# Kernel optimization log

Hardware: AMD Instinct MI355X
Metric: run time of the kernel (lower is better)

## Reference

```python
import jax, jax.numpy as jnp
import numpy as np

N, E, EP = 200000, 1600000, 1000000
D, H1, CH, XDIM, L = 64, 256, 128, 20, 3


def gelu(x):
    return jax.nn.gelu(x, approximate=False)  # torch default = exact erf GELU


def dyt(x, w, b, a):
    # DynamicTanh (channels_last): w * tanh(alpha * x) + b
    return w * jnp.tanh(a * x) + b


def graph_norm(x, w, b, ms, eps=1e-5):
    # PyG GraphNorm with a single graph (batch = all zeros)
    mean = jnp.mean(x, axis=0, keepdims=True)
    xc = x - ms * mean
    var = jnp.mean(xc * xc, axis=0, keepdims=True)
    return w * xc / jnp.sqrt(var + eps) + b


def setup_inputs() -> dict:
    key = jax.random.key(0)
    ks = iter(jax.random.split(key, 64))
    nrm = lambda shape, s: jax.random.normal(next(ks), shape, jnp.float32) * s
    d = {}
    d['x_res'] = nrm((N, D), 1.0)
    s = 1.0 / np.sqrt(D)
    d['Wl'] = nrm((L, D, D), s); d['bl'] = jnp.zeros((L, D)); d['Wr'] = nrm((L, D, D), s)
    d['gn_w'] = jnp.ones((L, D)); d['gn_b'] = jnp.zeros((L, D)); d['gn_ms'] = jnp.ones((L, D))
    d['dyt1_w'] = jnp.ones((L * D,)); d['dyt1_b'] = jnp.zeros((L * D,)); d['dyt1_a'] = jnp.full((1,), 0.5, jnp.float32)
    d['lin1_w'] = nrm((L * D, H1), 1.0 / np.sqrt(L * D)); d['lin1_b'] = jnp.zeros((H1,))
    d['lin2_w'] = nrm((H1, H1), 1.0 / np.sqrt(H1)); d['lin2_b'] = jnp.zeros((H1,))
    d['lin3_w'] = nrm((H1, D), 1.0 / np.sqrt(H1)); d['lin3_b'] = jnp.zeros((D,))
    d['dyt2_w'] = jnp.ones((D,)); d['dyt2_b'] = jnp.zeros((D,)); d['dyt2_a'] = jnp.full((1,), 0.5, jnp.float32)
    d['adyt1_w'] = jnp.ones((2 * D,)); d['adyt1_b'] = jnp.zeros((2 * D,)); d['adyt1_a'] = jnp.full((1,), 0.5, jnp.float32)
    d['aa1_w'] = nrm((2 * D, H1), 1.0 / np.sqrt(2 * D)); d['aa1_b'] = jnp.zeros((H1,))
    d['aa2_w'] = nrm((H1, H1), 1.0 / np.sqrt(H1)); d['aa2_b'] = jnp.zeros((H1,))
    d['aa3_w'] = nrm((H1, H1), 1.0 / np.sqrt(H1)); d['aa3_b'] = jnp.zeros((H1,))
    d['adyt2_w'] = jnp.ones((H1,)); d['adyt2_b'] = jnp.zeros((H1,)); d['adyt2_a'] = jnp.full((1,), 0.5, jnp.float32)
    d['aa4_w'] = nrm((H1, XDIM), 1.0 / np.sqrt(H1)); d['aa4_b'] = jnp.zeros((XDIM,))
    d['c1_w'] = nrm((2 * D, CH), 1.0 / np.sqrt(2 * D)); d['c1_b'] = jnp.zeros((CH,))
    d['c2_w'] = nrm((CH, CH), 1.0 / np.sqrt(CH)); d['c2_b'] = jnp.zeros((CH,))
    d['c3_w'] = nrm((CH, 1), 1.0 / np.sqrt(CH)); d['c3_b'] = jnp.zeros((1,))
    d['edge_index'] = jax.random.randint(next(ks), (2, E), 0, N, dtype=jnp.int64 if jax.config.jax_enable_x64 else jnp.int32).astype(jnp.int32)
    d['contact_pred_index'] = jax.random.randint(next(ks), (2, EP), 0, N).astype(jnp.int32)
    return d


def reference(x_res, Wl, bl, Wr, gn_w, gn_b, gn_ms, dyt1_w, dyt1_b, dyt1_a,
              lin1_w, lin1_b, lin2_w, lin2_b, lin3_w, lin3_b, dyt2_w, dyt2_b, dyt2_a,
              adyt1_w, adyt1_b, adyt1_a, aa1_w, aa1_b, aa2_w, aa2_b, aa3_w, aa3_b,
              adyt2_w, adyt2_b, adyt2_a, aa4_w, aa4_b,
              c1_w, c1_b, c2_w, c2_b, c3_w, c3_b, edge_index, contact_pred_index):
    n = x_res.shape[0]
    src, dst = edge_index[0], edge_index[1]
    inz = x_res  # dropout is identity in eval / p~0
    x = x_res
    # in-degree for SAGE mean aggregation (clamped to 1 like PyG)
    deg = jnp.maximum(jax.ops.segment_sum(jnp.ones_like(src, dtype=x.dtype), dst, num_segments=n), 1.0)[:, None]
    xs = []
    for i in range(Wl.shape[0]):
        prev = x
        agg = jax.ops.segment_sum(x[src], dst, num_segments=n) / deg  # [N, D] mean of neighbor messages
        h = agg @ Wl[i] + bl[i] + x @ Wr[i]                            # SAGEConv: lin_l(aggr) + lin_r(x_dst)
        h = gelu(h)
        h = graph_norm(h, gn_w[i], gn_b[i], gn_ms[i])
        if i > 0:
            h = h + prev  # residual from layer 1 onward
        x = h
        xs.append(x)
    z = jnp.concatenate(xs, axis=1)  # JumpingKnowledge 'cat' -> [N, 3*D]
    z = dyt(z, dyt1_w, dyt1_b, dyt1_a)
    z = gelu(z @ lin1_w + lin1_b)
    z = gelu(z @ lin2_w + lin2_b)
    z = gelu(z @ lin3_w + lin3_b)
    z = dyt(z, dyt2_w, dyt2_b, dyt2_a)
    z = z + inz                                   # residual=True
    z = z / (jnp.linalg.norm(z, axis=1, keepdims=True) + 1e-10)  # normalize=True
    dec_in = jnp.concatenate([inz, z], axis=1)    # [N, 2*D]
    a = dyt(dec_in, adyt1_w, adyt1_b, adyt1_a)
    a = gelu(a @ aa1_w + aa1_b)
    a = gelu(a @ aa2_w + aa2_b)
    a = gelu(a @ aa3_w + aa3_b)
    a = dyt(a, adyt2_w, adyt2_b, adyt2_a)
    aa = jax.nn.log_softmax(a @ aa4_w + aa4_b, axis=1)  # [N, 20]
    ci, cj = contact_pred_index[0], contact_pred_index[1]
    ce = jnp.concatenate([z[ci], z[cj]], axis=1)  # [EP, 2*D] gather
    ce = gelu(ce @ c1_w + c1_b)
    ce = gelu(ce @ c2_w + c2_b)
    edge_probs = jax.nn.sigmoid((ce @ c3_w + c3_b)[:, 0])  # [EP]
    return aa, edge_probs
```

## Files before the change

### kernel.cpp

```cpp
#include <hip/hip_runtime.h>
#include <cstdint>
#include <cstddef>

constexpr int Nn  = 200000;
constexpr int Ee  = 1600000;
constexpr int EPp = 1000000;

typedef __attribute__((ext_vector_type(8))) short bf8_t;
typedef __attribute__((ext_vector_type(4))) float f4_t;

__device__ inline unsigned short f2bf(float f) {
  union { float f; unsigned u; } v; v.f = f;
  unsigned r = v.u + 0x7FFFu + ((v.u >> 16) & 1u);
  return (unsigned short)(r >> 16);
}
__device__ inline float bf2f(unsigned short u) {
  union { unsigned u; float f; } v; v.u = ((unsigned)u) << 16;
  return v.f;
}
__device__ inline float gelu_f(float v) {
  float u = v * fmaf(0.0356774081f, v * v, 0.7978845608f);
  float r = __builtin_amdgcn_rcpf(__expf(u + u) + 1.0f);
  return fmaf(-v, r, v);
}
__device__ inline float dyt_f(float x, float s2, float w, float b) {
  float r = __builtin_amdgcn_rcpf(__expf(s2 * x) + 1.0f);
  return fmaf(w, fmaf(-2.0f, r, 1.0f), b);
}


__global__ __launch_bounds__(256) void k_degi(const int* __restrict__ dst,
                                              int* __restrict__ cnt, int E) {
  int i = blockIdx.x * 256 + threadIdx.x;
  if (i < E) atomicAdd(&cnt[dst[i]], 1);
}

__global__ __launch_bounds__(256) void k_rdeg(const int* __restrict__ cnt,
                                              float* __restrict__ rdeg, int n) {
  int i = blockIdx.x * 256 + threadIdx.x;
  if (i < n) rdeg[i] = 1.0f / (float)(cnt[i] > 1 ? cnt[i] : 1);
}

__global__ __launch_bounds__(256) void k_scan1(const int* __restrict__ in,
                                               int* __restrict__ out,
                                               int* __restrict__ bsum, int n) {
  __shared__ int sd[256];
  int t = threadIdx.x;
  int base = blockIdx.x * 1024 + t * 4;
  int v[4]; int ts = 0;
  #pragma unroll
  for (int j = 0; j < 4; ++j) { v[j] = (base + j < n) ? in[base + j] : 0; ts += v[j]; }
  sd[t] = ts; __syncthreads();
  for (int off = 1; off < 256; off <<= 1) {
    int x = (t >= off) ? sd[t - off] : 0;
    __syncthreads();
    sd[t] += x;
    __syncthreads();
  }
  int excl = sd[t] - ts;
  #pragma unroll
  for (int j = 0; j < 4; ++j) { if (base + j < n) out[base + j] = excl; excl += v[j]; }
  if (t == 255) bsum[blockIdx.x] = sd[255];
}

__global__ void k_scan2(int* bsum, int nb) {
  __shared__ int sd[256];
  int t = threadIdx.x;
  int v = (t < nb) ? bsum[t] : 0;
  sd[t] = v; __syncthreads();
  for (int off = 1; off < 256; off <<= 1) {
    int x = (t >= off) ? sd[t - off] : 0;
    __syncthreads();
    sd[t] += x;
    __syncthreads();
  }
  if (t < nb) bsum[t] = sd[t] - v;
}

__global__ __launch_bounds__(256) void k_scan3(const int* __restrict__ part,
                                               const int* __restrict__ bsum,
                                               int* __restrict__ rowptr,
                                               int* __restrict__ cursor,
                                               int n, int total) {
  int i = blockIdx.x * 256 + threadIdx.x;
  if (i == 0) rowptr[n] = total;
  if (i < n) { int v = part[i] + bsum[i >> 10]; rowptr[i] = v; cursor[i] = v; }
}

__global__ __launch_bounds__(256) void k_fill(const int* __restrict__ src,
                                              const int* __restrict__ dst,
                                              int* __restrict__ cursor,
                                              int* __restrict__ colidx, int E) {
  int e = blockIdx.x * 256 + threadIdx.x;
  if (e >= E) return;
  int pos = atomicAdd(&cursor[dst[e]], 1);
  colidx[pos] = src[e];
}

__global__ __launch_bounds__(256) void k_gather(const unsigned short* __restrict__ x, int ldx,
                                                const int* __restrict__ rowptr,
                                                const int* __restrict__ colidx,
                                                const float* __restrict__ rdeg,
                                                unsigned short* __restrict__ agg, int n) {
  int wave = threadIdx.x >> 6, lane = threadIdx.x & 63;
  int node = blockIdx.x * 4 + wave;
  if (node >= n) return;
  int grp = lane >> 3, c = (lane & 7) * 8;
  int r0 = rowptr[node], r1 = rowptr[node + 1];
  float s[8] = {0.f, 0.f, 0.f, 0.f, 0.f, 0.f, 0.f, 0.f};
  for (int j = r0 + grp; j < r1; j += 8) {
    bf8_t v = *(const bf8_t*)(x + (size_t)colidx[j] * ldx + c);
    #pragma unroll
    for (int jj = 0; jj < 8; ++jj) s[jj] += bf2f((unsigned short)v[jj]);
  }
  #pragma unroll
  for (int jj = 0; jj < 8; ++jj) {
    s[jj] += __shfl_xor(s[jj], 8, 64);
    s[jj] += __shfl_xor(s[jj], 16, 64);
    s[jj] += __shfl_xor(s[jj], 32, 64);
  }
  if (grp == 0) {
    float r = rdeg[node];
    bf8_t o;
    #pragma unroll
    for (int jj = 0; jj < 8; ++jj) o[jj] = (short)f2bf(s[jj] * r);
    *(bf8_t*)(agg + (size_t)node * 64 + c) = o;
  }
}


__global__ __launch_bounds__(256) void k_cvt(const float* __restrict__ in,
                                             unsigned short* __restrict__ out, int n) {
  int i = blockIdx.x * 256 + threadIdx.x;
  if (i < n) out[i] = f2bf(in[i]);
}

__global__ __launch_bounds__(256) void k_wt2(const float* __restrict__ W,
                                             unsigned short* __restrict__ Wt,
                                             int K, int N, int total) {
  int i = blockIdx.x * 256 + threadIdx.x;
  if (i >= total) return;
  int n = i / K, k = i - n * K;
  float v = (n < N) ? W[(size_t)k * N + n] : 0.f;
  Wt[i] = f2bf(v);
}

__global__ __launch_bounds__(256) void k_wt3(const float* __restrict__ W,
                                             unsigned short* __restrict__ Wt,
                                             int Np, int Nr, int total) {
  int i = blockIdx.x * 256 + threadIdx.x;
  if (i >= total) return;
  int kin = i & 31;
  int j = i >> 5;
  int n = j % Np, kb = j / Np;
  int k = kb * 32 + kin;
  float v = (n < Nr) ? W[(size_t)k * Nr + n] : 0.f;
  Wt[i] = f2bf(v);
}

__global__ __launch_bounds__(256) void k_wtsage(const float* __restrict__ Wl,
                                                const float* __restrict__ Wr,
                                                unsigned short* __restrict__ Wt) {
  int i = blockIdx.x * 256 + threadIdx.x;
  if (i >= 3 * 64 * 128) return;
  int l = i >> 13, r = i & 8191, n = r >> 7, k = r & 127;
  float v = (k < 64) ? Wl[l * 4096 + k * 64 + n] : Wr[l * 4096 + (k - 64) * 64 + n];
  Wt[i] = f2bf(v);
}

__global__ __launch_bounds__(256) void k_stats(const float* __restrict__ h,
                                               float* __restrict__ stats, int n) {
  int lane = threadIdx.x & 63, grp = threadIdx.x >> 6;
  float s = 0.f, s2 = 0.f;
  for (int r = blockIdx.x * 4 + grp; r < n; r += gridDim.x * 4) {
    float v = h[(size_t)r * 64 + lane];
    s += v; s2 += v * v;
  }
  __shared__ float l1[4][64], l2[4][64];
  l1[grp][lane] = s; l2[grp][lane] = s2;
  __syncthreads();
  if (grp == 0) {
    s  = l1[0][lane] + l1[1][lane] + l1[2][lane] + l1[3][lane];
    s2 = l2[0][lane] + l2[1][lane] + l2[2][lane] + l2[3][lane];
    atomicAdd(&stats[lane], s);
    atomicAdd(&stats[64 + lane], s2);
  }
}

__global__ void k_statfin(float* stats, const float* __restrict__ ms_, int n) {
  int d = threadIdx.x;
  if (d < 64) {
    float invn = 1.0f / (float)n;
    float m  = stats[d] * invn;
    float e2 = stats[64 + d] * invn;
    float ms = ms_[d];
    float var = e2 - (2.0f * ms - ms * ms) * m * m;
    stats[128 + d] = ms * m;
    stats[192 + d] = rsqrtf(var + 1e-5f);
  }
}

__global__ __launch_bounds__(256) void k_norm(const float* __restrict__ h,
                                              const float* __restrict__ stats,
                                              const float* __restrict__ w,
                                              const float* __restrict__ b,
                                              unsigned short* __restrict__ zcol,
                                              const unsigned short* __restrict__ prev, int n) {
  int i = blockIdx.x * 256 + threadIdx.x;
  if (i >= n * 64) return;
  int r = i >> 6, d = i & 63;
  float v = (h[i] - stats[128 + d]) * stats[192 + d] * w[d] + b[d];
  if (prev) v += bf2f(prev[(size_t)r * 192 + d]);
  zcol[(size_t)r * 192 + d] = f2bf(v);
}

template <int NT>
__global__ __launch_bounds__(256) void mgemm(
    const void* __restrict__ A1, int lda1,
    const void* __restrict__ A2, int lda2, int K1, int a_bf16,
    const unsigned short* __restrict__ Wt,
    const float* __restrict__ bias,
    void* __restrict__ Cout, int ldc, int c_bf16, int act,
    int M, int K, int N) {
  int lane = threadIdx.x & 63, wave = threadIdx.x >> 6;
  int quad = lane >> 4, col = lane & 15;
  int row0 = blockIdx.x * 128 + wave * 32;
  int n_base = blockIdx.y * NT * 16;

  f4_t acc[2][NT];
  #pragma unroll
  for (int mt = 0; mt < 2; ++mt)
    #pragma unroll
    for (int nt = 0; nt < NT; ++nt) acc[mt][nt] = (f4_t)0.f;

  int gm[2];
  gm[0] = row0 + col;      if (gm[0] >= M) gm[0] = M - 1;
  gm[1] = row0 + 16 + col; if (gm[1] >= M) gm[1] = M - 1;

  for (int kc0 = 0; kc0 < K; kc0 += 32) {
    int kc = kc0 + quad * 8;
    bf8_t a[2];
    #pragma unroll
    for (int mt = 0; mt < 2; ++mt) {
      const void* src; size_t off;
      if (kc < K1) { src = A1; off = (size_t)gm[mt] * lda1 + kc; }
      else         { src = A2; off = (size_t)gm[mt] * lda2 + kc - K1; }
      if (a_bf16) {
        a[mt] = *(const bf8_t*)((const unsigned short*)src + off);
      } else {
        const float* p = (const float*)src + off;
        float4 f0 = *(const float4*)p;
        float4 f1 = *(const float4*)(p + 4);
        float ff[8] = {f0.x, f0.y, f0.z, f0.w, f1.x, f1.y, f1.z, f1.w};
        #pragma unroll
        for (int j = 0; j < 8; ++j) a[mt][j] = (short)f2bf(ff[j]);
      }
    }
    #pragma unroll
    for (int nt = 0; nt < NT; ++nt) {
      bf8_t b = *(const bf8_t*)(Wt + (size_t)(n_base + nt * 16 + col) * K + kc);
      acc[0][nt] = __builtin_amdgcn_mfma_f32_16x16x32_bf16(a[0], b, acc[0][nt], 0, 0, 0);
      acc[1][nt] = __builtin_amdgcn_mfma_f32_16x16x32_bf16(a[1], b, acc[1][nt], 0, 0, 0);
    }
  }

  #pragma unroll
  for (int nt = 0; nt < NT; ++nt) {
    int n = n_base + nt * 16 + col;
    float bs = (bias && n < N) ? bias[n] : 0.f;
    #pragma unroll
    for (int mt = 0; mt < 2; ++mt)
      #pragma unroll
      for (int r = 0; r < 4; ++r) {
        int row = row0 + mt * 16 + quad * 4 + r;
        if (row >= M || n >= N) continue;
        float v = acc[mt][nt][r] + bs;
        if (act) v = gelu_f(v);
        if (c_bf16) ((unsigned short*)Cout)[(size_t)row * ldc + n] = f2bf(v);
        else        ((float*)Cout)[(size_t)row * ldc + n] = v;
      }
  }
}

template <int K, bool DYT>
__device__ inline void node_gemm(unsigned short (*H)[264],
                                 const unsigned short* __restrict__ W,
                                 const float* __restrict__ bias,
                                 int wave, int quad, int col,
                                 const float* __restrict__ a2w,
                                 const float* __restrict__ a2b,
                                 const float* __restrict__ aal) {
  constexpr int KS = K >> 5;
  f4_t acc[4][4];
  #pragma unroll
  for (int mt = 0; mt < 4; ++mt)
    #pragma unroll
    for (int nt = 0; nt < 4; ++nt) acc[mt][nt] = (f4_t)0.f;

  const unsigned short* wp = W + (size_t)(wave * 64 + col) * 32 + quad * 8;
  bf8_t bc[4];
  #pragma unroll
  for (int nt = 0; nt < 4; ++nt)
    bc[nt] = *(const bf8_t*)(wp + (size_t)(nt * 16) * 32);

  #pragma unroll 2
  for (int s = 0; s < KS; ++s) {
    bf8_t am[4];
    #pragma unroll
    for (int mt = 0; mt < 4; ++mt)
      am[mt] = *(const bf8_t*)&H[mt * 16 + col][s * 32 + quad * 8];
    bf8_t bn[4];
    if (s + 1 < KS) {
      #pragma unroll
      for (int nt = 0; nt < 4; ++nt)
        bn[nt] = *(const bf8_t*)(wp + (size_t)((s + 1) * 256 + nt * 16) * 32);
    }
    #pragma unroll
    for (int nt = 0; nt < 4; ++nt)
      #pragma unroll
      for (int mt = 0; mt < 4; ++mt)
        acc[mt][nt] = __builtin_amdgcn_mfma_f32_16x16x32_bf16(am[mt], bc[nt], acc[mt][nt], 0, 0, 0);
    if (s + 1 < KS) {
      #pragma unroll
      for (int nt = 0; nt < 4; ++nt) bc[nt] = bn[nt];
    }
  }
  __syncthreads();
  float sa = DYT ? (2.0f * aal[0]) : 0.f;
  #pragma unroll
  for (int nt = 0; nt < 4; ++nt) {
    int n = wave * 64 + nt * 16 + col;
    float bs = bias[n];
    float w_ = DYT ? a2w[n] : 0.f;
    float b_ = DYT ? a2b[n] : 0.f;
    #pragma unroll
    for (int mt = 0; mt < 4; ++mt)
      #pragma unroll
      for (int r4 = 0; r4 < 4; ++r4) {
        float v = gelu_f(acc[mt][nt][r4] + bs);
        if (DYT) v = dyt_f(v, sa, w_, b_);
        H[mt * 16 + quad * 4 + r4][n] = f2bf(v);
      }
  }
  __syncthreads();
}

__global__ __launch_bounds__(256, 3) void k_node(
    const unsigned short* __restrict__ z_bf,
    const float* __restrict__ x_res,
    const float* __restrict__ d1w, const float* __restrict__ d1b, const float* __restrict__ d1a,
    const unsigned short* __restrict__ wt1, const float* __restrict__ b1,
    const unsigned short* __restrict__ wt2, const float* __restrict__ b2,
    const unsigned short* __restrict__ wt3, const float* __restrict__ b3,
    const float* __restrict__ d2w, const float* __restrict__ d2b, const float* __restrict__ d2a,
    const float* __restrict__ a1w, const float* __restrict__ a1b, const float* __restrict__ a1a,
    const unsigned short* __restrict__ wa1, const float* __restrict__ ba1,
    const unsigned short* __restrict__ wa2, const float* __restrict__ ba2,
    const unsigned short* __restrict__ wa3, const float* __restrict__ ba3,
    const float* __restrict__ a2w, const float* __restrict__ a2b, const float* __restrict__ a2a,
    const unsigned short* __restrict__ wa4, const float* __restrict__ ba4,
    unsigned short* __restrict__ zn_bf,
    float* __restrict__ out, int M) {
  __shared__ unsigned short H[64][264];
  __shared__ float fscr[64 * 4 + 64];
  int t = threadIdx.x;
  int lane = t & 63, wave = t >> 6;
  int quad = lane >> 4, col = lane & 15;
  int brow = blockIdx.x * 64;

  {
    int row = t >> 2, part = t & 3;
    int gr = brow + row; if (gr >= M) gr = M - 1;
    const unsigned short* zp = z_bf + (size_t)gr * 192 + part * 48;
    float s1 = 2.0f * d1a[0];
    #pragma unroll
    for (int j = 0; j < 6; ++j) {
      bf8_t v = *(const bf8_t*)(zp + j * 8);
      int k0 = part * 48 + j * 8;
      #pragma unroll
      for (int jj = 0; jj < 8; ++jj) {
        float f = bf2f((unsigned short)v[jj]);
        v[jj] = (short)f2bf(dyt_f(f, s1, d1w[k0 + jj], d1b[k0 + jj]));
      }
      *(bf8_t*)&H[row][k0] = v;
    }
  }
  __syncthreads();

  node_gemm<192, false>(H, wt1, b1, wave, quad, col, nullptr, nullptr, nullptr);
  node_gemm<256, false>(H, wt2, b2, wave, quad, col, nullptr, nullptr, nullptr);

  {
    f4_t a3[4];
    #pragma unroll
    for (int mt = 0; mt < 4; ++mt) a3[mt] = (f4_t)0.f;
    const unsigned short* wp3 = wt3 + (size_t)(wave * 16 + col) * 32 + quad * 8;
    bf8_t bc = *(const bf8_t*)(wp3);
    #pragma unroll 2
    for (int s = 0; s < 8; ++s) {
      bf8_t am[4];
      #pragma unroll
      for (int mt = 0; mt < 4; ++mt)
        am[mt] = *(const bf8_t*)&H[mt * 16 + col][s * 32 + quad * 8];
      bf8_t bn;
      if (s + 1 < 8) bn = *(const bf8_t*)(wp3 + (size_t)((s + 1) * 64) * 32);
      #pragma unroll
      for (int mt = 0; mt < 4; ++mt)
        a3[mt] = __builtin_amdgcn_mfma_f32_16x16x32_bf16(am[mt], bc, a3[mt], 0, 0, 0);
      if (s + 1 < 8) bc = bn;
    }
    __syncthreads();
    float* fb = (float*)H;
    float s2d = 2.0f * d2a[0];
    int n = wave * 16 + col;
    float bsn = b3[n], wd = d2w[n], bd = d2b[n];
    #pragma unroll
    for (int mt = 0; mt < 4; ++mt)
      #pragma unroll
      for (int r4 = 0; r4 < 4; ++r4) {
        int row = mt * 16 + quad * 4 + r4;
        int gr = brow + row; if (gr >= M) gr = M - 1;
        float g = gelu_f(a3[mt][r4] + bsn);
        float x = x_res[(size_t)gr * 64 + n];
        fb[row * 66 + n] = dyt_f(g, s2d, wd, bd) + x;
      }
    __syncthreads();
    int row = t >> 2, q = t & 3;
    float vreg[16];
    float s2 = 0.f;
    #pragma unroll
    for (int c16 = 0; c16 < 16; ++c16) {
      vreg[c16] = fb[row * 66 + q * 16 + c16];
      s2 += vreg[c16] * vreg[c16];
    }
    fscr[row * 4 + q] = s2;
    __syncthreads();
    if (t < 64)
      fscr[256 + t] = 1.0f / (sqrtf(fscr[t * 4] + fscr[t * 4 + 1] + fscr[t * 4 + 2] + fscr[t * 4 + 3]) + 1e-10f);
    __syncthreads();
    float sa1 = 2.0f * a1a[0];
    float inv = fscr[256 + row];
    int gr = brow + row;
    int grc = (gr >= M) ? (M - 1) : gr;
    #pragma unroll
    for (int c16 = 0; c16 < 16; ++c16) {
      int c = q * 16 + c16;
      float zv = vreg[c16] * inv;
      if (gr < M) zn_bf[(size_t)gr * 64 + c] = f2bf(zv);
      float x = x_res[(size_t)grc * 64 + c];
      H[row][64 + c] = f2bf(dyt_f(zv, sa1, a1w[64 + c], a1b[64 + c]));
      H[row][c]      = f2bf(dyt_f(x,  sa1, a1w[c],      a1b[c]));
    }
    __syncthreads();
  }

  node_gemm<128, false>(H, wa1, ba1, wave, quad, col, nullptr, nullptr, nullptr);
  node_gemm<256, false>(H, wa2, ba2, wave, quad, col, nullptr, nullptr, nullptr);
  node_gemm<256, true >(H, wa3, ba3, wave, quad, col, a2w, a2b, a2a);

  {
    f4_t a4[2];
    a4[0] = (f4_t)0.f; a4[1] = (f4_t)0.f;
    const unsigned short* wp4 = wa4 + (size_t)col * 32 + quad * 8;
    bf8_t bc[2];
    bc[0] = *(const bf8_t*)(wp4);
    bc[1] = *(const bf8_t*)(wp4 + (size_t)(16) * 32);
    #pragma unroll 2
    for (int s = 0; s < 8; ++s) {
      bf8_t am = *(const bf8_t*)&H[wave * 16 + col][s * 32 + quad * 8];
      bf8_t bn[2];
      if (s + 1 < 8) {
        bn[0] = *(const bf8_t*)(wp4 + (size_t)((s + 1) * 32) * 32);
        bn[1] = *(const bf8_t*)(wp4 + (size_t)((s + 1) * 32 + 16) * 32);
      }
      #pragma unroll
      for (int nt = 0; nt < 2; ++nt)
        a4[nt] = __builtin_amdgcn_mfma_f32_16x16x32_bf16(am, bc[nt], a4[nt], 0, 0, 0);
      if (s + 1 < 8) { bc[0] = bn[0]; bc[1] = bn[1]; }
    }
    float val[2][4];
    #pragma unroll
    for (int nt = 0; nt < 2; ++nt) {
      int n = nt * 16 + col;
      float bsv = (n < 20) ? ba4[n] : 0.f;
      #pragma unroll
      for (int r4 = 0; r4 < 4; ++r4) val[nt][r4] = a4[nt][r4] + bsv;
    }
    bool v1 = (col < 4);
    #pragma unroll
    for (int r4 = 0; r4 < 4; ++r4) {
      float m = val[0][r4];
      if (v1) m = fmaxf(m, val[1][r4]);
      m = fmaxf(m, __shfl_xor(m, 1, 64));
      m = fmaxf(m, __shfl_xor(m, 2, 64));
      m = fmaxf(m, __shfl_xor(m, 4, 64));
      m = fmaxf(m, __shfl_xor(m, 8, 64));
      float se = __expf(val[0][r4] - m) + (v1 ? __expf(val[1][r4] - m) : 0.f);
      se += __shfl_xor(se, 1, 64);
      se += __shfl_xor(se, 2, 64);
      se += __shfl_xor(se, 4, 64);
      se += __shfl_xor(se, 8, 64);
      float ls = __logf(se) + m;
      int row = brow + wave * 16 + quad * 4 + r4;
      if (row < M) {
        out[(size_t)row * 20 + col] = val[0][r4] - ls;
        if (v1) out[(size_t)row * 20 + 16 + col] = val[1][r4] - ls;
      }
    }
  }
}

__global__ __launch_bounds__(256) void k_edge(
    const unsigned short* __restrict__ zn_bf,
    const int* __restrict__ ci, const int* __restrict__ cj,
    const unsigned short* __restrict__ w1t, const float* __restrict__ b1,
    const unsigned short* __restrict__ w2t, const float* __restrict__ b2,
    const float* __restrict__ w3, const float* __restrict__ b3,
    float* __restrict__ out, int M) {
  __shared__ unsigned short h1s[4][16][136];
  int lane = threadIdx.x & 63, wave = threadIdx.x >> 6;
  int quad = lane >> 4, col = lane & 15;
  unsigned short (*h1)[136] = h1s[wave];
  int ntiles = (M + 63) >> 6;
  float b3v = b3[0];

  int tile = blockIdx.x;
  bf8_t afrag[4];
  if (tile < ntiles) {
    int r = tile * 64 + wave * 16 + col; if (r >= M) r = M - 1;
    const unsigned short* p0 = zn_bf + (size_t)ci[r] * 64;
    const unsigned short* p1 = zn_bf + (size_t)cj[r] * 64;
    afrag[0] = *(const bf8_t*)(p0 + quad * 8);
    afrag[1] = *(const bf8_t*)(p0 + 32 + quad * 8);
    afrag[2] = *(const bf8_t*)(p1 + quad * 8);
    afrag[3] = *(const bf8_t*)(p1 + 32 + quad * 8);
  }

  for (; tile < ntiles; tile += gridDim.x) {
    f4_t acc[8];
    #pragma unroll
    for (int nt = 0; nt < 8; ++nt) acc[nt] = (f4_t)0.f;
    #pragma unroll
    for (int s = 0; s < 4; ++s) {
      int kf = s * 32 + quad * 8;
      #pragma unroll
      for (int nt = 0; nt < 8; ++nt) {
        bf8_t b = *(const bf8_t*)(w1t + (size_t)(nt * 16 + col) * 128 + kf);
        acc[nt] = __builtin_amdgcn_mfma_f32_16x16x32_bf16(afrag[s], b, acc[nt], 0, 0, 0);
      }
    }

    int nxt = tile + gridDim.x;
    bf8_t nfrag[4];
    bool has_next = (nxt < ntiles);
    if (has_next) {
      int r = nxt * 64 + wave * 16 + col; if (r >= M) r = M - 1;
      const unsigned short* p0 = zn_bf + (size_t)ci[r] * 64;
      const unsigned short* p1 = zn_bf + (size_t)cj[r] * 64;
      nfrag[0] = *(const bf8_t*)(p0 + quad * 8);
      nfrag[1] = *(const bf8_t*)(p0 + 32 + quad * 8);
      nfrag[2] = *(const bf8_t*)(p1 + quad * 8);
      nfrag[3] = *(const bf8_t*)(p1 + 32 + quad * 8);
    }

    #pragma unroll
    for (int nt = 0; nt < 8; ++nt) {
      float bs = b1[nt * 16 + col];
      #pragma unroll
      for (int r4 = 0; r4 < 4; ++r4)
        h1[quad * 4 + r4][nt * 16 + col] = f2bf(gelu_f(acc[nt][r4] + bs));
    }

    f4_t a2[8];
    #pragma unroll
    for (int nt = 0; nt < 8; ++nt) a2[nt] = (f4_t)0.f;
    #pragma unroll
    for (int s = 0; s < 4; ++s) {
      int kc = s * 32 + quad * 8;
      bf8_t a0 = *(const bf8_t*)&h1[col][kc];
      #pragma unroll
      for (int nt = 0; nt < 8; ++nt) {
        bf8_t b = *(const bf8_t*)(w2t + (size_t)(nt * 16 + col) * 128 + kc);
        a2[nt] = __builtin_amdgcn_mfma_f32_16x16x32_bf16(a0, b, a2[nt], 0, 0, 0);
      }
    }
    float p[4] = {0.f, 0.f, 0.f, 0.f};
    #pragma unroll
    for (int nt = 0; nt < 8; ++nt) {
      float bs = b2[nt * 16 + col];
      float wv = w3[nt * 16 + col];
      #pragma unroll
      for (int r4 = 0; r4 < 4; ++r4)
        p[r4] += gelu_f(a2[nt][r4] + bs) * wv;
    }
    #pragma unroll
    for (int r4 = 0; r4 < 4; ++r4) {
      float s = p[r4];
      s += __shfl_xor(s, 1, 64);
      s += __shfl_xor(s, 2, 64);
      s += __shfl_xor(s, 4, 64);
      s += __shfl_xor(s, 8, 64);
      if (col == 0) {
        int row = tile * 64 + wave * 16 + quad * 4 + r4;
        if (row < M) out[row] = __builtin_amdgcn_rcpf(1.0f + __expf(-(s + b3v)));
      }
    }

    if (has_next) {
      afrag[0] = nfrag[0]; afrag[1] = nfrag[1];
      afrag[2] = nfrag[2]; afrag[3] = nfrag[3];
    }
  }
}

extern "C" void kernel_launch(void* const* d_in, const int* in_sizes, int n_in,
                              void* d_out, int out_size, void* d_ws, size_t ws_size,
                              hipStream_t stream) {
  const float* x_res  = (const float*)d_in[0];
  const float* Wl     = (const float*)d_in[1];
  const float* bl     = (const float*)d_in[2];
  const float* Wr     = (const float*)d_in[3];
  const float* gn_w   = (const float*)d_in[4];
  const float* gn_b   = (const float*)d_in[5];
  const float* gn_ms  = (const float*)d_in[6];
  const float* dyt1_w = (const float*)d_in[7];
  const float* dyt1_b = (const float*)d_in[8];
  const float* dyt1_a = (const float*)d_in[9];
  const float* lin1_w = (const float*)d_in[10];
  const float* lin1_b = (const float*)d_in[11];
  const float* lin2_w = (const float*)d_in[12];
  const float* lin2_b = (const float*)d_in[13];
  const float* lin3_w = (const float*)d_in[14];
  const float* lin3_b = (const float*)d_in[15];
  const float* dyt2_w = (const float*)d_in[16];
  const float* dyt2_b = (const float*)d_in[17];
  const float* dyt2_a = (const float*)d_in[18];
  const float* adyt1_w = (const float*)d_in[19];
  const float* adyt1_b = (const float*)d_in[20];
  const float* adyt1_a = (const float*)d_in[21];
  const float* aa1_w  = (const float*)d_in[22];
  const float* aa1_b  = (const float*)d_in[23];
  const float* aa2_w  = (const float*)d_in[24];
  const float* aa2_b  = (const float*)d_in[25];
  const float* aa3_w  = (const float*)d_in[26];
  const float* aa3_b  = (const float*)d_in[27];
  const float* adyt2_w = (const float*)d_in[28];
  const float* adyt2_b = (const float*)d_in[29];
  const float* adyt2_a = (const float*)d_in[30];
  const float* aa4_w  = (const float*)d_in[31];
  const float* aa4_b  = (const float*)d_in[32];
  const float* c1_w   = (const float*)d_in[33];
  const float* c1_b   = (const float*)d_in[34];
  const float* c2_w   = (const float*)d_in[35];
  const float* c2_b   = (const float*)d_in[36];
  const float* c3_w   = (const float*)d_in[37];
  const float* c3_b   = (const float*)d_in[38];
  const int*   edge   = (const int*)d_in[39];
  const int*   contact = (const int*)d_in[40];

  const size_t N = (size_t)Nn;
  const size_t ws_floats = ws_size / 4;

  float* ws    = (float*)d_ws;
  float* rdeg  = ws;
  float* hbuf  = rdeg + N;
  unsigned short* z_bf  = (unsigned short*)(hbuf + 64 * N);
  unsigned short* zn_bf = z_bf + 192 * N;
  float* stats = (float*)(zn_bf + 64 * N);
  unsigned short* wt_sage = (unsigned short*)(stats + 256);
  unsigned short* wt_lin1 = wt_sage + 3 * 64 * 128;
  unsigned short* wt_lin2 = wt_lin1 + 256 * 192;
  unsigned short* wt_lin3 = wt_lin2 + 256 * 256;
  unsigned short* wt_aa1  = wt_lin3 + 64 * 256;
  unsigned short* wt_aa2  = wt_aa1 + 256 * 128;
  unsigned short* wt_aa3  = wt_aa2 + 256 * 256;
  unsigned short* wt_aa4  = wt_aa3 + 256 * 256;
  unsigned short* wt_c1   = wt_aa4 + 32 * 256;
  unsigned short* wt_c2   = wt_c1 + 128 * 128;
  unsigned short* wt_end  = wt_c2 + 128 * 128;
  float* pool  = (float*)((((uintptr_t)wt_end + 15) & ~(uintptr_t)15));
  const size_t persist = (size_t)(pool - ws);

  const size_t gnn_need = 32 * N + N + (N + 1) + N + (size_t)Ee + 256;
  if (ws_floats < persist + gnn_need) return;

  unsigned short* agg_bf = (unsigned short*)pool;
  int* cnt     = (int*)(pool + 32 * N);
  int* rowptr  = cnt + N;
  int* cursor  = rowptr + N + 1;
  int* colidx  = cursor + N;
  int* bsum    = colidx + Ee;

  const int* esrc = edge;
  const int* edst = edge + Ee;

  hipMemsetAsync(cnt, 0, N * sizeof(int), stream);
  k_degi<<<(Ee + 255) / 256, 256, 0, stream>>>(edst, cnt, Ee);
  k_rdeg<<<(Nn + 255) / 256, 256, 0, stream>>>(cnt, rdeg, Nn);
  const int nb = (Nn + 1023) / 1024;
  k_scan1<<<nb, 256, 0, stream>>>(cnt, cursor, bsum, Nn);
  k_scan2<<<1, 256, 0, stream>>>(bsum, nb);
  k_scan3<<<(Nn + 255) / 256, 256, 0, stream>>>(cursor, bsum, rowptr, cursor, Nn, Ee);
  k_fill<<<(Ee + 255) / 256, 256, 0, stream>>>(esrc, edst, cursor, colidx, Ee);

  k_wtsage<<<(3 * 64 * 128 + 255) / 256, 256, 0, stream>>>(Wl, Wr, wt_sage);
  k_wt3<<<(192 * 256 + 255) / 256, 256, 0, stream>>>(lin1_w, wt_lin1, 256, 256, 192 * 256);
  k_wt3<<<(256 * 256 + 255) / 256, 256, 0, stream>>>(lin2_w, wt_lin2, 256, 256, 256 * 256);
  k_wt3<<<(256 * 64 + 255) / 256, 256, 0, stream>>>(lin3_w, wt_lin3, 64, 64, 256 * 64);
  k_wt3<<<(128 * 256 + 255) / 256, 256, 0, stream>>>(aa1_w, wt_aa1, 256, 256, 128 * 256);
  k_wt3<<<(256 * 256 + 255) / 256, 256, 0, stream>>>(aa2_w, wt_aa2, 256, 256, 256 * 256);
  k_wt3<<<(256 * 256 + 255) / 256, 256, 0, stream>>>(aa3_w, wt_aa3, 256, 256, 256 * 256);
  k_wt3<<<(256 * 32 + 255) / 256, 256, 0, stream>>>(aa4_w, wt_aa4, 32, 20, 256 * 32);
  k_wt2<<<(128 * 128 + 255) / 256, 256, 0, stream>>>(c1_w, wt_c1, 128, 128, 128 * 128);
  k_wt2<<<(128 * 128 + 255) / 256, 256, 0, stream>>>(c2_w, wt_c2, 128, 128, 128 * 128);

  k_cvt<<<(int)((N * 64 + 255) / 256), 256, 0, stream>>>(x_res, zn_bf, (int)(N * 64));

  for (int l = 0; l < 3; ++l) {
    const unsigned short* xi = (l == 0) ? zn_bf : (z_bf + (size_t)(l - 1) * 64);
    int ldx = (l == 0) ? 64 : 192;
    hipMemsetAsync(stats, 0, 128 * sizeof(float), stream);
    k_gather<<<(Nn + 3) / 4, 256, 0, stream>>>(xi, ldx, rowptr, colidx, rdeg, agg_bf, Nn);
    mgemm<4><<<dim3((Nn + 127) / 128, 1), 256, 0, stream>>>(
        agg_bf, 64, xi, ldx, 64, 1,
        wt_sage + (size_t)l * 8192, bl + l * 64, hbuf, 64, 0, 1, Nn, 128, 64);
    k_stats<<<1024, 256, 0, stream>>>(hbuf, stats, Nn);
    k_statfin<<<1, 64, 0, stream>>>(stats, gn_ms + l * 64, Nn);
    k_norm<<<(Nn * 64) / 256, 256, 0, stream>>>(hbuf, stats, gn_w + l * 64, gn_b + l * 64,
                                                z_bf + (size_t)l * 64,
                                                (l > 0) ? (z_bf + (size_t)(l - 1) * 64) : nullptr, Nn);
  }

  k_node<<<(Nn + 63) / 64, 256, 0, stream>>>(
      z_bf, x_res,
      dyt1_w, dyt1_b, dyt1_a, wt_lin1, lin1_b, wt_lin2, lin2_b, wt_lin3, lin3_b,
      dyt2_w, dyt2_b, dyt2_a,
      adyt1_w, adyt1_b, adyt1_a, wt_aa1, aa1_b, wt_aa2, aa2_b, wt_aa3, aa3_b,
      adyt2_w, adyt2_b, adyt2_a, wt_aa4, aa4_b,
      zn_bf, (float*)d_out, Nn);

  float* eout = (float*)d_out + (size_t)Nn * 20;
  k_edge<<<2048, 256, 0, stream>>>(zn_bf, contact, contact + EPp,
      wt_c1, c1_b, wt_c2, c2_b, c3_w, c3_b, eout, EPp);
}
```

Before: 1.479 ms.

## Fuse GraphNorm stats into SAGE GEMM epilogue and merge setup kernels

The separate statistics pass over hbuf is replaced by per-column sum and sum-of-squares gathered in the GEMM epilogue. These use shared-memory atomics, then global atomics into per-layer stats slots that are zeroed once up front. The reciprocal-degree computation moves into the scan kernel, and the ten weight-transpose launches collapse into one kernel. This removes a full read of the 200k x 64 fp32 buffer per layer plus several launches and memsets, at the cost of atomic contention in the GEMM epilogue.

```diff
diff --git a/kernel.cpp b/kernel.cpp
--- a/kernel.cpp
+++ b/kernel.cpp
@@ -35,15 +35,10 @@
   if (i < E) atomicAdd(&cnt[dst[i]], 1);
 }
 
-__global__ __launch_bounds__(256) void k_rdeg(const int* __restrict__ cnt,
-                                              float* __restrict__ rdeg, int n) {
-  int i = blockIdx.x * 256 + threadIdx.x;
-  if (i < n) rdeg[i] = 1.0f / (float)(cnt[i] > 1 ? cnt[i] : 1);
-}
-
 __global__ __launch_bounds__(256) void k_scan1(const int* __restrict__ in,
                                                int* __restrict__ out,
-                                               int* __restrict__ bsum, int n) {
+                                               int* __restrict__ bsum,
+                                               float* __restrict__ rdeg, int n) {
   __shared__ int sd[256];
   int t = threadIdx.x;
   int base = blockIdx.x * 1024 + t * 4;
@@ -59,7 +54,13 @@
   }
   int excl = sd[t] - ts;
   #pragma unroll
-  for (int j = 0; j < 4; ++j) { if (base + j < n) out[base + j] = excl; excl += v[j]; }
+  for (int j = 0; j < 4; ++j) {
+    if (base + j < n) {
+      out[base + j] = excl;
+      rdeg[base + j] = 1.0f / (float)(v[j] > 1 ? v[j] : 1);
+    }
+    excl += v[j];
+  }
   if (t == 255) bsum[blockIdx.x] = sd[255];
 }
 
@@ -135,21 +136,9 @@
   if (i < n) out[i] = f2bf(in[i]);
 }
 
-__global__ __launch_bounds__(256) void k_wt2(const float* __restrict__ W,
-                                             unsigned short* __restrict__ Wt,
-                                             int K, int N, int total) {
-  int i = blockIdx.x * 256 + threadIdx.x;
-  if (i >= total) return;
-  int n = i / K, k = i - n * K;
-  float v = (n < N) ? W[(size_t)k * N + n] : 0.f;
-  Wt[i] = f2bf(v);
-}
-
-__global__ __launch_bounds__(256) void k_wt3(const float* __restrict__ W,
-                                             unsigned short* __restrict__ Wt,
-                                             int Np, int Nr, int total) {
-  int i = blockIdx.x * 256 + threadIdx.x;
-  if (i >= total) return;
+__device__ inline void wt3_elem(const float* __restrict__ W,
+                                unsigned short* __restrict__ Wt,
+                                int Np, int Nr, int i) {
   int kin = i & 31;
   int j = i >> 5;
   int n = j % Np, kb = j / Np;
@@ -157,34 +146,44 @@
   float v = (n < Nr) ? W[(size_t)k * Nr + n] : 0.f;
   Wt[i] = f2bf(v);
 }
-
-__global__ __launch_bounds__(256) void k_wtsage(const float* __restrict__ Wl,
-                                                const float* __restrict__ Wr,
-                                                unsigned short* __restrict__ Wt) {
+__device__ inline void wt2_elem(const float* __restrict__ W,
+                                unsigned short* __restrict__ Wt,
+                                int K, int N, int i) {
+  int n = i / K, k = i - n * K;
+  float v = (n < N) ? W[(size_t)k * N + n] : 0.f;
+  Wt[i] = f2bf(v);
+}
+
+__global__ __launch_bounds__(256) void k_wtall(
+    const float* __restrict__ Wl, const float* __restrict__ Wr,
+    const float* __restrict__ lin1_w, const float* __restrict__ lin2_w,
+    const float* __restrict__ lin3_w,
+    const float* __restrict__ aa1_w, const float* __restrict__ aa2_w,
+    const float* __restrict__ aa3_w, const float* __restrict__ aa4_w,
+    const float* __restrict__ c1_w, const float* __restrict__ c2_w,
+    unsigned short* __restrict__ wt_sage,
+    unsigned short* __restrict__ wt_lin1, unsigned short* __restrict__ wt_lin2,
+    unsigned short* __restrict__ wt_lin3,
+    unsigned short* __restrict__ wt_aa1, unsigned short* __restrict__ wt_aa2,
+    unsigned short* __restrict__ wt_aa3, unsigned short* __restrict__ wt_aa4,
+    unsigned short* __restrict__ wt_c1, unsigned short* __restrict__ wt_c2) {
   int i = blockIdx.x * 256 + threadIdx.x;
-  if (i >= 3 * 64 * 128) return;
-  int l = i >> 13, r = i & 8191, n = r >> 7, k = r & 127;
-  float v = (k < 64) ? Wl[l * 4096 + k * 64 + n] : Wr[l * 4096 + (k - 64) * 64 + n];
-  Wt[i] = f2bf(v);
-}
-
-__global__ __launch_bounds__(256) void k_stats(const float* __restrict__ h,
-                                               float* __restrict__ stats, int n) {
-  int lane = threadIdx.x & 63, grp = threadIdx.x >> 6;
-  float s = 0.f, s2 = 0.f;
-  for (int r = blockIdx.x * 4 + grp; r < n; r += gridDim.x * 4) {
-    float v = h[(size_t)r * 64 + lane];
-    s += v; s2 += v * v;
-  }
-  __shared__ float l1[4][64], l2[4][64];
-  l1[grp][lane] = s; l2[grp][lane] = s2;
-  __syncthreads();
-  if (grp == 0) {
-    s  = l1[0][lane] + l1[1][lane] + l1[2][lane] + l1[3][lane];
-    s2 = l2[0][lane] + l2[1][lane] + l2[2][lane] + l2[3][lane];
-    atomicAdd(&stats[lane], s);
-    atomicAdd(&stats[64 + lane], s2);
-  }
+  if (i < 24576) {
+    int l = i >> 13, r = i & 8191, n = r >> 7, k = r & 127;
+    float v = (k < 64) ? Wl[l * 4096 + k * 64 + n] : Wr[l * 4096 + (k - 64) * 64 + n];
+    wt_sage[i] = f2bf(v);
+    return;
+  }
+  i -= 24576;
+  if (i < 49152) { wt3_elem(lin1_w, wt_lin1, 256, 256, i); return; }  i -= 49152;
+  if (i < 65536) { wt3_elem(lin2_w, wt_lin2, 256, 256, i); return; }  i -= 65536;
+  if (i < 16384) { wt3_elem(lin3_w, wt_lin3, 64, 64, i);   return; }  i -= 16384;
+  if (i < 32768) { wt3_elem(aa1_w, wt_aa1, 256, 256, i);   return; }  i -= 32768;
+  if (i < 65536) { wt3_elem(aa2_w, wt_aa2, 256, 256, i);   return; }  i -= 65536;
+  if (i < 65536) { wt3_elem(aa3_w, wt_aa3, 256, 256, i);   return; }  i -= 65536;
+  if (i < 8192)  { wt3_elem(aa4_w, wt_aa4, 32, 20, i);     return; }  i -= 8192;
+  if (i < 16384) { wt2_elem(c1_w, wt_c1, 128, 128, i);     return; }  i -= 16384;
+  if (i < 16384) { wt2_elem(c2_w, wt_c2, 128, 128, i);     return; }
 }
 
 __global__ void k_statfin(float* stats, const float* __restrict__ ms_, int n) {
@@ -221,11 +220,18 @@
     const unsigned short* __restrict__ Wt,
     const float* __restrict__ bias,
     void* __restrict__ Cout, int ldc, int c_bf16, int act,
+    float* __restrict__ stats_out,
     int M, int K, int N) {
   int lane = threadIdx.x & 63, wave = threadIdx.x >> 6;
   int quad = lane >> 4, col = lane & 15;
   int row0 = blockIdx.x * 128 + wave * 32;
   int n_base = blockIdx.y * NT * 16;
+
+  __shared__ float ls[128];
+  if (stats_out) {
+    if (threadIdx.x < 128) ls[threadIdx.x] = 0.f;
+    __syncthreads();
+  }
 
   f4_t acc[2][NT];
   #pragma unroll
@@ -268,6 +274,7 @@
   for (int nt = 0; nt < NT; ++nt) {
     int n = n_base + nt * 16 + col;
     float bs = (bias && n < N) ? bias[n] : 0.f;
+    float sa = 0.f, s2a = 0.f;
     #pragma unroll
     for (int mt = 0; mt < 2; ++mt)
       #pragma unroll
@@ -276,9 +283,18 @@
         if (row >= M || n >= N) continue;
         float v = acc[mt][nt][r] + bs;
         if (act) v = gelu_f(v);
+        sa += v; s2a += v * v;
         if (c_bf16) ((unsigned short*)Cout)[(size_t)row * ldc + n] = f2bf(v);
         else        ((float*)Cout)[(size_t)row * ldc + n] = v;
       }
+    if (stats_out && n < N) {
+      atomicAdd(&ls[n & 63], sa);
+      atomicAdd(&ls[64 + (n & 63)], s2a);
+    }
+  }
+  if (stats_out) {
+    __syncthreads();
+    if (threadIdx.x < 128) atomicAdd(&stats_out[threadIdx.x], ls[threadIdx.x]);
   }
 }
 
@@ -667,7 +683,7 @@
   unsigned short* z_bf  = (unsigned short*)(hbuf + 64 * N);
   unsigned short* zn_bf = z_bf + 192 * N;
   float* stats = (float*)(zn_bf + 64 * N);
-  unsigned short* wt_sage = (unsigned short*)(stats + 256);
+  unsigned short* wt_sage = (unsigned short*)(stats + 768);
   unsigned short* wt_lin1 = wt_sage + 3 * 64 * 128;
   unsigned short* wt_lin2 = wt_lin1 + 256 * 192;
   unsigned short* wt_lin3 = wt_lin2 + 256 * 256;
@@ -695,38 +711,31 @@
   const int* edst = edge + Ee;
 
   hipMemsetAsync(cnt, 0, N * sizeof(int), stream);
+  hipMemsetAsync(stats, 0, 768 * sizeof(float), stream);
   k_degi<<<(Ee + 255) / 256, 256, 0, stream>>>(edst, cnt, Ee);
-  k_rdeg<<<(Nn + 255) / 256, 256, 0, stream>>>(cnt, rdeg, Nn);
   const int nb = (Nn + 1023) / 1024;
-  k_scan1<<<nb, 256, 0, stream>>>(cnt, cursor, bsum, Nn);
+  k_scan1<<<nb, 256, 0, stream>>>(cnt, cursor, bsum, rdeg, Nn);
   k_scan2<<<1, 256, 0, stream>>>(bsum, nb);
   k_scan3<<<(Nn + 255) / 256, 256, 0, stream>>>(cursor, bsum, rowptr, cursor, Nn, Ee);
   k_fill<<<(Ee + 255) / 256, 256, 0, stream>>>(esrc, edst, cursor, colidx, Ee);
 
-  k_wtsage<<<(3 * 64 * 128 + 255) / 256, 256, 0, stream>>>(Wl, Wr, wt_sage);
-  k_wt3<<<(192 * 256 + 255) / 256, 256, 0, stream>>>(lin1_w, wt_lin1, 256, 256, 192 * 256);
-  k_wt3<<<(256 * 256 + 255) / 256, 256, 0, stream>>>(lin2_w, wt_lin2, 256, 256, 256 * 256);
-  k_wt3<<<(256 * 64 + 255) / 256, 256, 0, stream>>>(lin3_w, wt_lin3, 64, 64, 256 * 64);
-  k_wt3<<<(128 * 256 + 255) / 256, 256, 0, stream>>>(aa1_w, wt_aa1, 256, 256, 128 * 256);
-  k_wt3<<<(256 * 256 + 255) / 256, 256, 0, stream>>>(aa2_w, wt_aa2, 256, 256, 256 * 256);
-  k_wt3<<<(256 * 256 + 255) / 256, 256, 0, stream>>>(aa3_w, wt_aa3, 256, 256, 256 * 256);
-  k_wt3<<<(256 * 32 + 255) / 256, 256, 0, stream>>>(aa4_w, wt_aa4, 32, 20, 256 * 32);
-  k_wt2<<<(128 * 128 + 255) / 256, 256, 0, stream>>>(c1_w, wt_c1, 128, 128, 128 * 128);
-  k_wt2<<<(128 * 128 + 255) / 256, 256, 0, stream>>>(c2_w, wt_c2, 128, 128, 128 * 128);
+  k_wtall<<<(360448 + 255) / 256, 256, 0, stream>>>(
+      Wl, Wr, lin1_w, lin2_w, lin3_w, aa1_w, aa2_w, aa3_w, aa4_w, c1_w, c2_w,
+      wt_sage, wt_lin1, wt_lin2, wt_lin3, wt_aa1, wt_aa2, wt_aa3, wt_aa4,
+      wt_c1, wt_c2);
 
   k_cvt<<<(int)((N * 64 + 255) / 256), 256, 0, stream>>>(x_res, zn_bf, (int)(N * 64));
 
   for (int l = 0; l < 3; ++l) {
     const unsigned short* xi = (l == 0) ? zn_bf : (z_bf + (size_t)(l - 1) * 64);
     int ldx = (l == 0) ? 64 : 192;
-    hipMemsetAsync(stats, 0, 128 * sizeof(float), stream);
+    float* stats_l = stats + (size_t)l * 256;
     k_gather<<<(Nn + 3) / 4, 256, 0, stream>>>(xi, ldx, rowptr, colidx, rdeg, agg_bf, Nn);
     mgemm<4><<<dim3((Nn + 127) / 128, 1), 256, 0, stream>>>(
         agg_bf, 64, xi, ldx, 64, 1,
-        wt_sage + (size_t)l * 8192, bl + l * 64, hbuf, 64, 0, 1, Nn, 128, 64);
-    k_stats<<<1024, 256, 0, stream>>>(hbuf, stats, Nn);
-    k_statfin<<<1, 64, 0, stream>>>(stats, gn_ms + l * 64, Nn);
-    k_norm<<<(Nn * 64) / 256, 256, 0, stream>>>(hbuf, stats, gn_w + l * 64, gn_b + l * 64,
+        wt_sage + (size_t)l * 8192, bl + l * 64, hbuf, 64, 0, 1, stats_l, Nn, 128, 64);
+    k_statfin<<<1, 64, 0, stream>>>(stats_l, gn_ms + l * 64, Nn);
+    k_norm<<<(Nn * 64) / 256, 256, 0, stream>>>(hbuf, stats_l, gn_w + l * 64, gn_b + l * 64,
                                                 z_bf + (size_t)l * 64,
                                                 (l > 0) ? (z_bf + (size_t)(l - 1) * 64) : nullptr, Nn);
   }
```

Result: no change. 1.451 ms (-1.9%).
